# Optimization experiments

Measured on AMD Instinct MI355X. Metric: run time of the kernel, lower is better.

The kernel has to match this reference:

```python
import jax, jax.numpy as jnp
import numpy as np

N_BITS = 14
L = 1 << N_BITS
B, C_IN, C_OUT = 32, 32, 64

def _neigh_idx():
    # (L, n_bits): index j flipped at bit b -> j ^ (1<<b)
    s = jnp.arange(L)
    return jnp.stack([s ^ (1 << b) for b in range(N_BITS)], axis=1)

def setup_inputs() -> dict:
    key = jax.random.key(0)
    k1, k2, k3, k4 = jax.random.split(key, 4)
    x = jax.random.normal(k1, (B, C_IN, L), dtype=jnp.float32)
    w_self = jnp.ones((), dtype=jnp.float32)
    w_bits = jax.random.normal(k2, (N_BITS,), dtype=jnp.float32) * 0.1
    # Conv1d(kernel_size=1) weight squeezed to (C_out, C_in)
    mix_w = jax.random.normal(k3, (C_OUT, C_IN), dtype=jnp.float32) * (1.0 / np.sqrt(C_IN))
    mix_b = jax.random.normal(k4, (C_OUT,), dtype=jnp.float32) * 0.01
    return {"x": x, "w_self": w_self, "w_bits": w_bits, "mix_w": mix_w, "mix_b": mix_b}

def reference(x, w_self, w_bits, mix_w, mix_b):
    n_bits = w_bits.shape[0]
    idx = _neigh_idx()                          # (L, n_bits), int32
    xn = x[:, :, idx]                           # (B, C, L, n_bits) XOR-neighbor gather
    neigh_sum = jnp.einsum('bclk,k->bcl', xn, w_bits)
    y = w_self * x + neigh_sum
    y = y / (1.0 + n_bits)                      # agg == 'mean'
    # 1x1 conv mix: (B,C,L) x (C_out,C_in) -> (B,C_out,L)
    return jnp.einsum('bcl,oc->bol', y, mix_w) + mix_b[None, :, None]
```

## Files before the change

### kernel.cpp

```cpp
#include <hip/hip_runtime.h>

#define TILE  256
#define CIN   32
#define COUT  64
#define LSIZE 16384
#define NBITS 14

typedef float vfloat4 __attribute__((ext_vector_type(4)));

__global__ __launch_bounds__(256, 4)
void hamming_fused(const float* __restrict__ x,
                   const float* __restrict__ w_self,
                   const float* __restrict__ w_bits,
                   const float* __restrict__ mix_w,
                   const float* __restrict__ mix_b,
                   float* __restrict__ out)
{
    __shared__ float xs[CIN][TILE];
    __shared__ float mws[CIN][COUT];

    const int tid = threadIdx.x;

    const int d    = blockIdx.x;
    const int xcd  = d & 7;
    const int j    = d >> 3;
    const int b    = xcd * 4 + (j >> 6);
    const int tile = j & 63;
    const int base = tile * TILE;
    const float* xb = x + (size_t)b * CIN * LSIZE;

    #pragma unroll
    for (int i = 0; i < (CIN * COUT) / 256; ++i) {
        int g = tid + i * 256;
        int o = g >> 5, c = g & 31;
        mws[c][o] = mix_w[g];
    }

    #pragma unroll
    for (int i = 0; i < (CIN * TILE) / (256 * 4); ++i) {
        int idx = tid + i * 256;
        int r  = idx >> 6;
        int c4 = (idx & 63) << 2;
        *(float4*)&xs[r][c4] =
            *(const float4*)(xb + (size_t)r * LSIZE + base + c4);
    }
    __syncthreads();

    const float ws = w_self[0];
    float wb[NBITS];
    #pragma unroll
    for (int k = 0; k < NBITS; ++k) wb[k] = w_bits[k];

    const int t    = tid;
    const int gcol = base + t;
    float yreg[CIN];

    #pragma unroll
    for (int c0 = 0; c0 < CIN; c0 += 8) {
        float pf[8][6];
        #pragma unroll
        for (int cc = 0; cc < 8; ++cc) {
            const float* xr = xb + (size_t)(c0 + cc) * LSIZE;
            #pragma unroll
            for (int k = 0; k < 6; ++k)
                pf[cc][k] = xr[gcol ^ (TILE << k)];
        }
        #pragma unroll
        for (int cc = 0; cc < 8; ++cc) {
            int c = c0 + cc;
            float a = ws * xs[c][t];
            #pragma unroll
            for (int k = 0; k < 8; ++k)
                a += wb[k] * xs[c][t ^ (1 << k)];
            #pragma unroll
            for (int k = 0; k < 6; ++k)
                a += wb[8 + k] * pf[cc][k];
            yreg[c] = a * (1.0f / 15.0f);
        }
    }
    __syncthreads();

    #pragma unroll
    for (int c = 0; c < CIN; ++c) xs[c][t] = yreg[c];
    __syncthreads();

    const int tx   = tid & 63;
    const int ty   = tid >> 6;
    const int colb = tx << 2;
    const int o0   = ty * 16;

    float4 acc[16];
    #pragma unroll
    for (int jj = 0; jj < 16; ++jj) {
        float bias = mix_b[o0 + jj];
        acc[jj] = make_float4(bias, bias, bias, bias);
    }

    #pragma unroll 4
    for (int c = 0; c < CIN; ++c) {
        float4 yv = *(float4*)&xs[c][colb];
        #pragma unroll
        for (int j4 = 0; j4 < 4; ++j4) {
            float4 m = *(float4*)&mws[c][o0 + j4 * 4];
            acc[j4*4+0].x += m.x * yv.x; acc[j4*4+0].y += m.x * yv.y;
            acc[j4*4+0].z += m.x * yv.z; acc[j4*4+0].w += m.x * yv.w;
            acc[j4*4+1].x += m.y * yv.x; acc[j4*4+1].y += m.y * yv.y;
            acc[j4*4+1].z += m.y * yv.z; acc[j4*4+1].w += m.y * yv.w;
            acc[j4*4+2].x += m.z * yv.x; acc[j4*4+2].y += m.z * yv.y;
            acc[j4*4+2].z += m.z * yv.z; acc[j4*4+2].w += m.z * yv.w;
            acc[j4*4+3].x += m.w * yv.x; acc[j4*4+3].y += m.w * yv.y;
            acc[j4*4+3].z += m.w * yv.z; acc[j4*4+3].w += m.w * yv.w;
        }
    }

    float* ob = out + (size_t)b * COUT * LSIZE;
    #pragma unroll
    for (int jj = 0; jj < 16; ++jj) {
        vfloat4 v; v.x = acc[jj].x; v.y = acc[jj].y; v.z = acc[jj].z; v.w = acc[jj].w;
        vfloat4* p = (vfloat4*)(ob + (size_t)(o0 + jj) * LSIZE + base + colb);
        __builtin_nontemporal_store(v, p);
    }
}

extern "C" void kernel_launch(void* const* d_in, const int* in_sizes, int n_in,
                              void* d_out, int out_size, void* d_ws, size_t ws_size,
                              hipStream_t stream) {
    const float* x      = (const float*)d_in[0];
    const float* w_self = (const float*)d_in[1];
    const float* w_bits = (const float*)d_in[2];
    const float* mix_w  = (const float*)d_in[3];
    const float* mix_b  = (const float*)d_in[4];
    float* out = (float*)d_out;

    hamming_fused<<<dim3(2048), 256, 0, stream>>>(x, w_self, w_bits, mix_w, mix_b, out);
}
```

Measured before the change: 210.5 us.

## Vectorize XOR-neighbor aggregation with float4 per thread over channel groups

Each thread now computes four adjacent columns for eight channels, instead of one column for all 32 channels. The global neighbor gathers become float4 loads and the low-bit neighbors come from shuffling within one float4 read from LDS. Because each thread writes back to exactly the rows it read, one barrier is removed. The mix-weight LDS rows are padded to 68 and launch bounds drop to 3 waves per SIMD, which trades occupancy for more registers.

Result: slower. 217.3 us (+3.2%).

```diff
diff --git a/kernel.cpp b/kernel.cpp
--- a/kernel.cpp
+++ b/kernel.cpp
@@ -5,10 +5,11 @@
 #define COUT  64
 #define LSIZE 16384
 #define NBITS 14
+#define MWPAD 68
 
 typedef float vfloat4 __attribute__((ext_vector_type(4)));
 
-__global__ __launch_bounds__(256, 4)
+__global__ __launch_bounds__(256, 3)
 void hamming_fused(const float* __restrict__ x,
                    const float* __restrict__ w_self,
                    const float* __restrict__ w_bits,
@@ -17,7 +18,7 @@
                    float* __restrict__ out)
 {
     __shared__ float xs[CIN][TILE];
-    __shared__ float mws[CIN][COUT];
+    __shared__ float mws[CIN][MWPAD];
 
     const int tid = threadIdx.x;
 
@@ -30,14 +31,13 @@
     const float* xb = x + (size_t)b * CIN * LSIZE;
 
     #pragma unroll
-    for (int i = 0; i < (CIN * COUT) / 256; ++i) {
+    for (int i = 0; i < 8; ++i) {
         int g = tid + i * 256;
-        int o = g >> 5, c = g & 31;
-        mws[c][o] = mix_w[g];
+        mws[g & 31][g >> 5] = mix_w[g];
     }
 
     #pragma unroll
-    for (int i = 0; i < (CIN * TILE) / (256 * 4); ++i) {
+    for (int i = 0; i < 8; ++i) {
         int idx = tid + i * 256;
         int r  = idx >> 6;
         int c4 = (idx & 63) << 2;
@@ -51,43 +51,58 @@
     #pragma unroll
     for (int k = 0; k < NBITS; ++k) wb[k] = w_bits[k];
 
-    const int t    = tid;
-    const int gcol = base + t;
-    float yreg[CIN];
+    const int tx   = tid & 63;
+    const int grp  = tid >> 6;
+    const int colb = tx << 2;
+    const int c0   = grp * 8;
+    const int gb   = base + colb;
+
+    float4 yreg[8];
+    #pragma unroll
+    for (int cc = 0; cc < 8; ++cc) {
+        const int c = c0 + cc;
+        const float* xr = xb + (size_t)c * LSIZE;
+
+        float4 g0 = *(const float4*)(xr + (gb ^ 256));
+        float4 g1 = *(const float4*)(xr + (gb ^ 512));
+        float4 g2 = *(const float4*)(xr + (gb ^ 1024));
+        float4 g3 = *(const float4*)(xr + (gb ^ 2048));
+        float4 g4 = *(const float4*)(xr + (gb ^ 4096));
+        float4 g5 = *(const float4*)(xr + (gb ^ 8192));
+
+        float4 s = *(float4*)&xs[c][colb];
+        float4 a;
+        a.x = ws * s.x + wb[0] * s.y + wb[1] * s.z;
+        a.y = ws * s.y + wb[0] * s.x + wb[1] * s.w;
+        a.z = ws * s.z + wb[0] * s.w + wb[1] * s.x;
+        a.w = ws * s.w + wb[0] * s.z + wb[1] * s.y;
+
+        #pragma unroll
+        for (int k = 2; k < 8; ++k) {
+            float4 tp = *(float4*)&xs[c][colb ^ (1 << k)];
+            a.x += wb[k] * tp.x;
+            a.y += wb[k] * tp.y;
+            a.z += wb[k] * tp.z;
+            a.w += wb[k] * tp.w;
+        }
+
+        a.x += wb[8]*g0.x + wb[9]*g1.x + wb[10]*g2.x + wb[11]*g3.x + wb[12]*g4.x + wb[13]*g5.x;
+        a.y += wb[8]*g0.y + wb[9]*g1.y + wb[10]*g2.y + wb[11]*g3.y + wb[12]*g4.y + wb[13]*g5.y;
+        a.z += wb[8]*g0.z + wb[9]*g1.z + wb[10]*g2.z + wb[11]*g3.z + wb[12]*g4.z + wb[13]*g5.z;
+        a.w += wb[8]*g0.w + wb[9]*g1.w + wb[10]*g2.w + wb[11]*g3.w + wb[12]*g4.w + wb[13]*g5.w;
+
+        yreg[cc].x = a.x * (1.0f / 15.0f);
+        yreg[cc].y = a.y * (1.0f / 15.0f);
+        yreg[cc].z = a.z * (1.0f / 15.0f);
+        yreg[cc].w = a.w * (1.0f / 15.0f);
+    }
 
     #pragma unroll
-    for (int c0 = 0; c0 < CIN; c0 += 8) {
-        float pf[8][6];
-        #pragma unroll
-        for (int cc = 0; cc < 8; ++cc) {
-            const float* xr = xb + (size_t)(c0 + cc) * LSIZE;
-            #pragma unroll
-            for (int k = 0; k < 6; ++k)
-                pf[cc][k] = xr[gcol ^ (TILE << k)];
-        }
-        #pragma unroll
-        for (int cc = 0; cc < 8; ++cc) {
-            int c = c0 + cc;
-            float a = ws * xs[c][t];
-            #pragma unroll
-            for (int k = 0; k < 8; ++k)
-                a += wb[k] * xs[c][t ^ (1 << k)];
-            #pragma unroll
-            for (int k = 0; k < 6; ++k)
-                a += wb[8 + k] * pf[cc][k];
-            yreg[c] = a * (1.0f / 15.0f);
-        }
-    }
+    for (int cc = 0; cc < 8; ++cc)
+        *(float4*)&xs[c0 + cc][colb] = yreg[cc];
     __syncthreads();
 
-    #pragma unroll
-    for (int c = 0; c < CIN; ++c) xs[c][t] = yreg[c];
-    __syncthreads();
-
-    const int tx   = tid & 63;
-    const int ty   = tid >> 6;
-    const int colb = tx << 2;
-    const int o0   = ty * 16;
+    const int o0 = grp * 16;
 
     float4 acc[16];
     #pragma unroll
```
